# Kernel tuning notes

Measured on AMD Instinct MI355X. Metric: run time of the kernel, lower is better.

The kernel has to match this reference:

```python
import jax, jax.numpy as jnp
import numpy as np

EPS = 1e-6
H = 16  # num_heads

def _ln(x):
    mu = jnp.mean(x, axis=-1, keepdims=True)
    var = jnp.mean(jnp.square(x - mu), axis=-1, keepdims=True)
    return (x - mu) / jnp.sqrt(var + EPS)

def _mod(x, shift, scale):  # shift/scale: [B,D]
    return x * (1.0 + scale[:, None, :]) + shift[:, None, :]

def _heads(x, qkv_w, qkv_b):
    B, N, C = x.shape
    hd = C // H
    qkv = (x @ qkv_w + qkv_b).reshape(B, N, 3, H, hd).transpose(2, 0, 3, 1, 4)
    return qkv[0], qkv[1], qkv[2]  # each [B,H,N,hd]

def _attend(q, k, v):
    sc = (q.shape[-1]) ** -0.5
    a = jax.nn.softmax(jnp.einsum('bhnd,bhmd->bhnm', q, k) * sc, axis=-1)
    o = jnp.einsum('bhnm,bhmd->bhnd', a, v)
    B, h, N, hd = o.shape
    return o.transpose(0, 2, 1, 3).reshape(B, N, h * hd)

def _mha(x, qkv_w, qkv_b, proj_w, proj_b):
    q, k, v = _heads(x, qkv_w, qkv_b)
    return _attend(q, k, v) @ proj_w + proj_b

def setup_inputs() -> dict:
    key = jax.random.key(0)
    ks = jax.random.split(key, 16)
    B, T, D = 2, 2048, 1024
    Dh = 4 * D
    s = 0.02
    return {
        'x': jax.random.normal(ks[0], (B, T, D), jnp.float32),
        'c': jax.random.normal(ks[1], (B, 2, D), jnp.float32),
        'attn_qkv_w': jax.random.normal(ks[2], (D, 3 * D), jnp.float32) * s,
        'attn_qkv_b': jnp.zeros((3 * D,), jnp.float32),
        'attn_proj_w': jax.random.normal(ks[3], (D, D), jnp.float32) * s,
        'attn_proj_b': jnp.zeros((D,), jnp.float32),
        'crs_qkv_w': jax.random.normal(ks[4], (D, 3 * D), jnp.float32) * s,
        'crs_qkv_b': jnp.zeros((3 * D,), jnp.float32),
        'crs_proj_w': jax.random.normal(ks[5], (D, D), jnp.float32) * s,
        'crs_proj_b': jnp.zeros((D,), jnp.float32),
        'mlp_fc1_w': jax.random.normal(ks[6], (D, Dh), jnp.float32) * s,
        'mlp_fc1_b': jnp.zeros((Dh,), jnp.float32),
        'mlp_fc2_w': jax.random.normal(ks[7], (Dh, D), jnp.float32) * s,
        'mlp_fc2_b': jnp.zeros((D,), jnp.float32),
        'ada_w': jax.random.normal(ks[8], (D, 9 * D), jnp.float32) * s,
        'ada_b': jnp.zeros((9 * D,), jnp.float32),
    }

def reference(x, c, attn_qkv_w, attn_qkv_b, attn_proj_w, attn_proj_b,
              crs_qkv_w, crs_qkv_b, crs_proj_w, crs_proj_b,
              mlp_fc1_w, mlp_fc1_b, mlp_fc2_w, mlp_fc2_b, ada_w, ada_b):
    # adaLN-zero modulation: SiLU + Linear -> 9 chunks of [B,2,D]
    mod = jax.nn.silu(c) @ ada_w + ada_b
    (sh_msa, sc_msa, g_msa, sh_mca, sc_mca, g_mca,
     sh_mlp, sc_mlp, g_mlp) = jnp.split(mod, 9, axis=2)
    B, T, D = x.shape
    h = T // 2
    x0, x1 = x[:, :h], x[:, h:]
    # self-attention on each half with its own shift/scale/gate
    x0 = x0 + g_msa[:, 0][:, None, :] * _mha(_mod(_ln(x0), sh_msa[:, 0], sc_msa[:, 0]),
                                             attn_qkv_w, attn_qkv_b, attn_proj_w, attn_proj_b)
    x1 = x1 + g_msa[:, 1][:, None, :] * _mha(_mod(_ln(x1), sh_msa[:, 1], sc_msa[:, 1]),
                                             attn_qkv_w, attn_qkv_b, attn_proj_w, attn_proj_b)
    # two-way cross-attention
    xm = _mod(_ln(x0), sh_mca[:, 0], sc_mca[:, 0])
    ym = _mod(_ln(x1), sh_mca[:, 1], sc_mca[:, 1])
    qx, kx, vx = _heads(xm, crs_qkv_w, crs_qkv_b)
    qy, ky, vy = _heads(ym, crs_qkv_w, crs_qkv_b)
    ox = _attend(qx, ky, vy) @ crs_proj_w + crs_proj_b
    oy = _attend(qy, kx, vx) @ crs_proj_w + crs_proj_b
    x = x + jnp.concatenate((g_mca[:, 0][:, None, :] * ox,
                             g_mca[:, 1][:, None, :] * oy), axis=1)
    # gated MLP on each half
    def mlp(z):
        return jax.nn.gelu(z @ mlp_fc1_w + mlp_fc1_b, approximate=True) @ mlp_fc2_w + mlp_fc2_b
    m0 = mlp(_mod(_ln(x[:, :h]), sh_mlp[:, 0], sc_mlp[:, 0]))
    m1 = mlp(_mod(_ln(x[:, h:]), sh_mlp[:, 1], sc_mlp[:, 1]))
    x = x + jnp.concatenate((g_mlp[:, 0][:, None, :] * m0,
                             g_mlp[:, 1][:, None, :] * m1), axis=1)
    return x
```

## Files before the change

kernel.cpp:

```cpp
#include <hip/hip_runtime.h>
#include <hip/hip_bf16.h>

#define BB 2
#define TT 2048
#define DD 1024
#define NH 16
#define HALF 1024
#define DHID 4096
#define ND9 9216
#define ROWS (BB*TT)

using bf16 = __hip_bfloat16;
typedef short bf16x8 __attribute__((ext_vector_type(8)));
typedef float f32x4 __attribute__((ext_vector_type(4)));
typedef unsigned short u16;

__device__ __forceinline__ float bits2f(u16 b){ return __uint_as_float(((unsigned)b) << 16); }
__device__ __forceinline__ u16 fb(float v){
    unsigned u = __float_as_uint(v);
    u += 0x7fffu + ((u >> 16) & 1u);
    return (u16)(u >> 16);
}
__device__ __forceinline__ u16 fbh(float v){
    bf16 b = __float2bfloat16(v);
    return *(u16*)&b;
}
__device__ __forceinline__ float fexp2(float x){
#if __has_builtin(__builtin_amdgcn_exp2f)
    return __builtin_amdgcn_exp2f(x);
#else
    return exp2f(x);
#endif
}
__device__ __forceinline__ void gl_lds16(const u16* g, u16* l) {
    __builtin_amdgcn_global_load_lds(
        (const __attribute__((address_space(1))) unsigned int*)g,
        (__attribute__((address_space(3))) unsigned int*)l, 16, 0, 0);
}

__global__ void ada_part(const float* __restrict__ c, const float* __restrict__ ada_w,
                         float* __restrict__ part) {
    __shared__ float sc_[4][64];
    int s = blockIdx.y;
    int k0 = s * 64;
    int n0 = blockIdx.x * 1024 + threadIdx.x * 4;
    {
        int r = threadIdx.x >> 6, k = threadIdx.x & 63;
        float v = c[r*DD + k0 + k];
        sc_[r][k] = v / (1.f + __expf(-v));
    }
    __syncthreads();
    float4 a0 = {0,0,0,0}, a1 = {0,0,0,0}, a2 = {0,0,0,0}, a3 = {0,0,0,0};
    for (int k = 0; k < 64; ++k) {
        float4 wv = *(const float4*)&ada_w[(size_t)(k0 + k)*ND9 + n0];
        float s0 = sc_[0][k], s1 = sc_[1][k], s2 = sc_[2][k], s3 = sc_[3][k];
        a0.x += s0*wv.x; a0.y += s0*wv.y; a0.z += s0*wv.z; a0.w += s0*wv.w;
        a1.x += s1*wv.x; a1.y += s1*wv.y; a1.z += s1*wv.z; a1.w += s1*wv.w;
        a2.x += s2*wv.x; a2.y += s2*wv.y; a2.z += s2*wv.z; a2.w += s2*wv.w;
        a3.x += s3*wv.x; a3.y += s3*wv.y; a3.z += s3*wv.z; a3.w += s3*wv.w;
    }
    *(float4*)&part[((size_t)(s*4 + 0))*ND9 + n0] = a0;
    *(float4*)&part[((size_t)(s*4 + 1))*ND9 + n0] = a1;
    *(float4*)&part[((size_t)(s*4 + 2))*ND9 + n0] = a2;
    *(float4*)&part[((size_t)(s*4 + 3))*ND9 + n0] = a3;
}

__global__ void ada_reduce(const float* __restrict__ part, const float* __restrict__ ada_b,
                           float* __restrict__ mod) {
    int g = blockIdx.x * 1024 + threadIdx.x * 4;
    int r = g / ND9, n = g - r*ND9;
    float4 acc = *(const float4*)&ada_b[n];
    #pragma unroll
    for (int s = 0; s < 16; ++s) {
        float4 p = *(const float4*)&part[((size_t)(s*4 + r))*ND9 + n];
        acc.x += p.x; acc.y += p.y; acc.z += p.z; acc.w += p.w;
    }
    *(float4*)&mod[(size_t)r*ND9 + n] = acc;
}

__global__ void resid_ln(const float* __restrict__ src, const u16* __restrict__ gv,
                         const float* __restrict__ mod, int jshift, int jscale,
                         float* __restrict__ dstf, bf16* __restrict__ y) {
    int row = blockIdx.x;
    int b = row / TT, t = row % TT;
    int cz = (t >= HALF) ? 1 : 0;
    const float* mp = mod + (size_t)(b*2 + cz) * ND9;
    int tid = threadIdx.x;
    int w = tid >> 6, lane = tid & 63;
    int d0 = tid * 4;
    float4 s = *(const float4*)&src[(size_t)row*DD + d0];
    float v[4] = {s.x, s.y, s.z, s.w};
    if (gv) {
        ushort4 g = *(const ushort4*)&gv[(size_t)row*DD + d0];
        v[0] += bits2f(g.x); v[1] += bits2f(g.y); v[2] += bits2f(g.z); v[3] += bits2f(g.w);
    }
    if (dstf) *(float4*)&dstf[(size_t)row*DD + d0] = (float4){v[0], v[1], v[2], v[3]};
    float sum = v[0]+v[1]+v[2]+v[3];
    float ssq = v[0]*v[0]+v[1]*v[1]+v[2]*v[2]+v[3]*v[3];
    #pragma unroll
    for (int o = 32; o > 0; o >>= 1) {
        sum += __shfl_down(sum, o);
        ssq += __shfl_down(ssq, o);
    }
    __shared__ float wsum[4], wssq[4];
    if (lane == 0) { wsum[w] = sum; wssq[w] = ssq; }
    __syncthreads();
    float sall = (wsum[0]+wsum[1]) + (wsum[2]+wsum[3]);
    float qall = (wssq[0]+wssq[1]) + (wssq[2]+wssq[3]);
    float mean = sall * (1.f/DD);
    float var = qall * (1.f/DD) - mean*mean;
    float rstd = rsqrtf(var + 1e-6f);
    float4 sh = *(const float4*)&mp[jshift*DD + d0];
    float4 sc = *(const float4*)&mp[jscale*DD + d0];
    ushort4 o4;
    o4.x = fb((v[0]-mean)*rstd*(1.f+sc.x) + sh.x);
    o4.y = fb((v[1]-mean)*rstd*(1.f+sc.y) + sh.y);
    o4.z = fb((v[2]-mean)*rstd*(1.f+sc.z) + sh.z);
    o4.w = fb((v[3]-mean)*rstd*(1.f+sc.w) + sh.w);
    *(ushort4*)((u16*)y + (size_t)row*DD + d0) = o4;
}

__global__ void transpose_w(const float* __restrict__ W, u16* __restrict__ Wt, int K, int N) {
    __shared__ float T[32][33];
    int n0 = blockIdx.x * 32, k0 = blockIdx.y * 32;
    int lx = threadIdx.x & 31, ly = threadIdx.x >> 5;
    #pragma unroll
    for (int i = 0; i < 4; ++i)
        T[ly + i*8][lx] = W[(size_t)(k0 + ly + i*8)*N + n0 + lx];
    __syncthreads();
    #pragma unroll
    for (int i = 0; i < 4; ++i) {
        int n = ly + i*8;
        Wt[(size_t)(n0 + n)*K + k0 + lx] = fb(T[lx][n]);
    }
}

__global__ void vtrans(const u16* __restrict__ qkv, u16* __restrict__ vt) {
    __shared__ u16 T[64][72];
    int kt = blockIdx.y;
    int gh = blockIdx.x;
    int tid = threadIdx.x;
    int key = tid >> 2, c8 = (tid & 3) * 16;
    const u16* src = qkv + (size_t)((gh >> 4)*1024 + kt*64 + key)*3072 + 2048 + (gh & 15)*64 + c8;
    *(uint4*)&T[key][c8]     = *(const uint4*)src;
    *(uint4*)&T[key][c8 + 8] = *(const uint4*)(src + 8);
    __syncthreads();
    int d = tid >> 2, kc = (tid & 3) * 16;
    u16 tmp[16];
    #pragma unroll
    for (int i = 0; i < 16; ++i) tmp[i] = T[kc + i][d];
    u16* dst = vt + ((size_t)gh*64 + d)*1024 + kt*64 + kc;
    *(uint4*)&dst[0] = *(const uint4*)&tmp[0];
    *(uint4*)&dst[8] = *(const uint4*)&tmp[8];
}

__device__ __forceinline__ void epi_store(u16* out, int o_off, int N, int mm, int n, float v,
                                          const float* mod, int jg, int epi) {
    if (epi == 0) {
        out[(size_t)(mm - o_off)*N + n] = fb(v);
    } else if (epi == 1) {
        float z = 0.7978845608028654f*(v + 0.044715f*v*v*v);
        out[(size_t)(mm - o_off)*N + n] = fb(v / (1.f + __expf(-2.f*z)));
    } else {
        int brow = mm / TT, tt2 = mm % TT;
        int cz = (tt2 >= HALF) ? 1 : 0;
        const float* mp = mod + (size_t)(brow*2 + cz)*ND9 + (size_t)jg*DD;
        if (epi == 3) {
            out[(size_t)(mm - o_off)*N + n] = fb(mp[n]*v);
        } else {
            float* of = (float*)out;
            size_t idx = (size_t)(mm - o_off)*N + n;
            of[idx] += mp[n]*v;
        }
    }
}

__global__ __launch_bounds__(256, 2) void gemm_mfma(
    const u16* __restrict__ A, const u16* __restrict__ Wt, const float* __restrict__ bias,
    u16* __restrict__ out, const float* __restrict__ mod, int jg,
    int m_base, int a_off, int o_off, int K, int N, int epi)
{
    __shared__ u16 As[128*64];
    __shared__ u16 Bs[128*64];
    int tid = threadIdx.x;
    int w = tid >> 6, lane = tid & 63;
    int quad = lane >> 4, l16 = lane & 15;
    int m0 = m_base + blockIdx.y * 128;
    int n0 = blockIdx.x * 128;
    int wr = (w & 1) * 64, wc = (w >> 1) * 64;

    f32x4 acc[4][4];
    #pragma unroll
    for (int i = 0; i < 4; ++i)
        #pragma unroll
        for (int j = 0; j < 4; ++j) acc[i][j] = (f32x4){0.f,0.f,0.f,0.f};

    const u16* Ag = A + (size_t)(m0 - a_off) * K;
    const u16* Bg = Wt + (size_t)n0 * K;
    int srow = lane >> 3;
    int scol = (((lane & 7) ^ ((lane >> 3) & 7))) * 8;
    int xsw = (l16 & 7);

    for (int k0 = 0; k0 < K; k0 += 64) {
        #pragma unroll
        for (int c = 0; c < 4; ++c) {
            int ch = w*4 + c;
            gl_lds16(Ag + (size_t)(ch*8 + srow)*K + k0 + scol, As + ch*512);
            gl_lds16(Bg + (size_t)(ch*8 + srow)*K + k0 + scol, Bs + ch*512);
        }
        __syncthreads();
        #pragma unroll
        for (int kk = 0; kk < 2; ++kk) {
            int pc = ((kk*4 + quad) ^ xsw) * 8;
            bf16x8 af[4], bfr[4];
            #pragma unroll
            for (int i = 0; i < 4; ++i) af[i] = *(const bf16x8*)&As[(wr + i*16 + l16)*64 + pc];
            #pragma unroll
            for (int j = 0; j < 4; ++j) bfr[j] = *(const bf16x8*)&Bs[(wc + j*16 + l16)*64 + pc];
            #pragma unroll
            for (int i = 0; i < 4; ++i)
                #pragma unroll
                for (int j = 0; j < 4; ++j)
                    acc[i][j] = __builtin_amdgcn_mfma_f32_16x16x32_bf16(af[i], bfr[j], acc[i][j], 0, 0, 0);
        }
        __syncthreads();
    }

    #pragma unroll
    for (int i = 0; i < 4; ++i)
        #pragma unroll
        for (int r = 0; r < 4; ++r) {
            int mm = m0 + wr + i*16 + quad*4 + r;
            #pragma unroll
            for (int j = 0; j < 4; ++j) {
                int n = n0 + wc + j*16 + l16;
                epi_store(out, o_off, N, mm, n, acc[i][j][r] + bias[n], mod, jg, epi);
            }
        }
}

__global__ __launch_bounds__(256, 2) void gemm64(
    const u16* __restrict__ A, const u16* __restrict__ Wt, const float* __restrict__ bias,
    u16* __restrict__ out, const float* __restrict__ mod, int jg,
    int m_base, int a_off, int o_off, int K, int N, int epi)
{
    __shared__ u16 As[64*64];
    __shared__ u16 Bs[128*64];
    int tid = threadIdx.x;
    int w = tid >> 6, lane = tid & 63;
    int quad = lane >> 4, l16 = lane & 15;
    int m0 = m_base + blockIdx.y * 64;
    int n0 = blockIdx.x * 128;

    f32x4 acc[4][2];
    #pragma unroll
    for (int i = 0; i < 4; ++i)
        #pragma unroll
        for (int j = 0; j < 2; ++j) acc[i][j] = (f32x4){0.f,0.f,0.f,0.f};

    const u16* Ag = A + (size_t)(m0 - a_off) * K;
    const u16* Bg = Wt + (size_t)n0 * K;
    int srow = lane >> 3;
    int scol = (((lane & 7) ^ ((lane >> 3) & 7))) * 8;
    int xsw = (l16 & 7);

    for (int k0 = 0; k0 < K; k0 += 64) {
        #pragma unroll
        for (int c = 0; c < 2; ++c) {
            int ch = w*2 + c;
            gl_lds16(Ag + (size_t)(ch*8 + srow)*K + k0 + scol, As + ch*512);
        }
        #pragma unroll
        for (int c = 0; c < 4; ++c) {
            int ch = w*4 + c;
            gl_lds16(Bg + (size_t)(ch*8 + srow)*K + k0 + scol, Bs + ch*512);
        }
        __syncthreads();
        #pragma unroll
        for (int kk = 0; kk < 2; ++kk) {
            int pc = ((kk*4 + quad) ^ xsw) * 8;
            bf16x8 af[4], bfr[2];
            #pragma unroll
            for (int i = 0; i < 4; ++i) af[i] = *(const bf16x8*)&As[(i*16 + l16)*64 + pc];
            #pragma unroll
            for (int j = 0; j < 2; ++j) bfr[j] = *(const bf16x8*)&Bs[(w*32 + j*16 + l16)*64 + pc];
            #pragma unroll
            for (int i = 0; i < 4; ++i)
                #pragma unroll
                for (int j = 0; j < 2; ++j)
                    acc[i][j] = __builtin_amdgcn_mfma_f32_16x16x32_bf16(af[i], bfr[j], acc[i][j], 0, 0, 0);
        }
        __syncthreads();
    }

    #pragma unroll
    for (int i = 0; i < 4; ++i)
        #pragma unroll
        for (int r = 0; r < 4; ++r) {
            int mm = m0 + i*16 + quad*4 + r;
            #pragma unroll
            for (int j = 0; j < 2; ++j) {
                int n = n0 + w*32 + j*16 + l16;
                epi_store(out, o_off, N, mm, n, acc[i][j][r] + bias[n], mod, jg, epi);
            }
        }
}

__global__ __launch_bounds__(256) void attn_mfma(const u16* __restrict__ qkv,
                                                 const u16* __restrict__ vt,
                                                 u16* __restrict__ attn_out, int kv_swap) {
    __shared__ u16 Ks[2][64][72];
    __shared__ u16 Vs[2][64][72];
    __shared__ u16 Ps[4][16][72];
    int head = blockIdx.x, qt = blockIdx.y, bh = blockIdx.z;
    int kvbh = kv_swap ? (bh ^ 1) : bh;
    int tid = threadIdx.x;
    int w = tid >> 6, lane = tid & 63;
    int quad = lane >> 4, l16 = lane & 15;
    int qrow0 = bh*1024 + qt*64 + w*16;

    const u16* qp = qkv + (size_t)(qrow0 + l16)*3072 + head*64;
    bf16x8 qa0 = *(const bf16x8*)(qp + quad*8);
    bf16x8 qa1 = *(const bf16x8*)(qp + 32 + quad*8);

    f32x4 oacc[4];
    #pragma unroll
    for (int i = 0; i < 4; ++i) oacc[i] = (f32x4){0.f,0.f,0.f,0.f};
    float mst = -3e38f, lst = 0.f;

    int skey = tid >> 2, sc8 = (tid & 3) * 16;
    const u16* kbase = qkv + (size_t)(kvbh*1024 + skey)*3072 + 1024 + head*64 + sc8;
    const u16* vbase = vt + ((size_t)(kvbh*16 + head)*64 + skey)*1024 + sc8;

    uint4 kr0 = *(const uint4*)kbase;
    uint4 kr1 = *(const uint4*)(kbase + 8);
    uint4 vr0 = *(const uint4*)vbase;
    uint4 vr1 = *(const uint4*)(vbase + 8);
    *(uint4*)&Ks[0][skey][sc8]     = kr0;
    *(uint4*)&Ks[0][skey][sc8 + 8] = kr1;
    *(uint4*)&Vs[0][skey][sc8]     = vr0;
    *(uint4*)&Vs[0][skey][sc8 + 8] = vr1;
    __syncthreads();

    const float SSC = 0.125f * 1.4426950408889634f;
    int cur = 0;
    for (int kt = 0; kt < 16; ++kt) {
        if (kt < 15) {
            const u16* kp = kbase + (size_t)(kt + 1)*64*3072;
            kr0 = *(const uint4*)kp;
            kr1 = *(const uint4*)(kp + 8);
            const u16* vp = vbase + (kt + 1)*64;
            vr0 = *(const uint4*)vp;
            vr1 = *(const uint4*)(vp + 8);
        }

        f32x4 sacc[4];
        #pragma unroll
        for (int nt = 0; nt < 4; ++nt) sacc[nt] = (f32x4){0.f,0.f,0.f,0.f};
        __builtin_amdgcn_s_setprio(1);
        #pragma unroll
        for (int nt = 0; nt < 4; ++nt) {
            bf16x8 kb0 = *(const bf16x8*)&Ks[cur][nt*16 + l16][quad*8];
            bf16x8 kb1 = *(const bf16x8*)&Ks[cur][nt*16 + l16][32 + quad*8];
            sacc[nt] = __builtin_amdgcn_mfma_f32_16x16x32_bf16(kb0, qa0, sacc[nt], 0, 0, 0);
            sacc[nt] = __builtin_amdgcn_mfma_f32_16x16x32_bf16(kb1, qa1, sacc[nt], 0, 0, 0);
        }
        __builtin_amdgcn_s_setprio(0);

        float sv[4][4];
        float tm = -3e38f;
        #pragma unroll
        for (int nt = 0; nt < 4; ++nt)
            #pragma unroll
            for (int r = 0; r < 4; ++r) {
                sv[nt][r] = sacc[nt][r] * SSC;
                tm = fmaxf(tm, sv[nt][r]);
            }
        tm = fmaxf(tm, __shfl_xor(tm, 16));
        tm = fmaxf(tm, __shfl_xor(tm, 32));
        if (!__all(tm <= mst + 11.5f)) {
            float mnew = fmaxf(mst, tm);
            float alpha = fexp2(mst - mnew);
            lst *= alpha;
            #pragma unroll
            for (int dt = 0; dt < 4; ++dt)
                #pragma unroll
                for (int r = 0; r < 4; ++r) oacc[dt][r] *= alpha;
            mst = mnew;
        }
        float ls = 0.f;
        #pragma unroll
        for (int nt = 0; nt < 4; ++nt) {
            float p0 = fexp2(sv[nt][0] - mst), p1 = fexp2(sv[nt][1] - mst);
            float p2 = fexp2(sv[nt][2] - mst), p3 = fexp2(sv[nt][3] - mst);
            ls += (p0 + p1) + (p2 + p3);
            ushort4 pk = {fbh(p0), fbh(p1), fbh(p2), fbh(p3)};
            *(ushort4*)&Ps[w][l16][nt*16 + quad*4] = pk;
        }
        ls += __shfl_xor(ls, 16);
        ls += __shfl_xor(ls, 32);
        lst += ls;

        bf16x8 pa0 = *(const bf16x8*)&Ps[w][l16][quad*8];
        bf16x8 pa1 = *(const bf16x8*)&Ps[w][l16][32 + quad*8];
        __builtin_amdgcn_s_setprio(1);
        #pragma unroll
        for (int dt = 0; dt < 4; ++dt) {
            bf16x8 vb0 = *(const bf16x8*)&Vs[cur][dt*16 + l16][quad*8];
            bf16x8 vb1 = *(const bf16x8*)&Vs[cur][dt*16 + l16][32 + quad*8];
            oacc[dt] = __builtin_amdgcn_mfma_f32_16x16x32_bf16(vb0, pa0, oacc[dt], 0, 0, 0);
            oacc[dt] = __builtin_amdgcn_mfma_f32_16x16x32_bf16(vb1, pa1, oacc[dt], 0, 0, 0);
        }
        __builtin_amdgcn_s_setprio(0);

        if (kt < 15) {
            int nxt = cur ^ 1;
            *(uint4*)&Ks[nxt][skey][sc8]     = kr0;
            *(uint4*)&Ks[nxt][skey][sc8 + 8] = kr1;
            *(uint4*)&Vs[nxt][skey][sc8]     = vr0;
            *(uint4*)&Vs[nxt][skey][sc8 + 8] = vr1;
            __syncthreads();
            cur = nxt;
        }
    }
    float rl = 1.f / lst;
    #pragma unroll
    for (int dt = 0; dt < 4; ++dt) {
        ushort4 o4 = {fbh(oacc[dt][0]*rl), fbh(oacc[dt][1]*rl),
                      fbh(oacc[dt][2]*rl), fbh(oacc[dt][3]*rl)};
        *(ushort4*)&attn_out[(size_t)(qrow0 + l16)*DD + head*64 + dt*16 + quad*4] = o4;
    }
}

extern "C" void kernel_launch(void* const* d_in, const int* in_sizes, int n_in,
                              void* d_out, int out_size, void* d_ws, size_t ws_size,
                              hipStream_t stream) {
    const float* x          = (const float*)d_in[0];
    const float* c          = (const float*)d_in[1];
    const float* attn_qkv_w = (const float*)d_in[2];
    const float* attn_qkv_b = (const float*)d_in[3];
    const float* attn_proj_w= (const float*)d_in[4];
    const float* attn_proj_b= (const float*)d_in[5];
    const float* crs_qkv_w  = (const float*)d_in[6];
    const float* crs_qkv_b  = (const float*)d_in[7];
    const float* crs_proj_w = (const float*)d_in[8];
    const float* crs_proj_b = (const float*)d_in[9];
    const float* fc1_w      = (const float*)d_in[10];
    const float* fc1_b      = (const float*)d_in[11];
    const float* fc2_w      = (const float*)d_in[12];
    const float* fc2_b      = (const float*)d_in[13];
    const float* ada_w      = (const float*)d_in[14];
    const float* ada_b      = (const float*)d_in[15];
    float* out = (float*)d_out;

    char* ws = (char*)d_ws;
    float* mod = (float*)ws;
    char* R1   = ws + (256u<<10);
    char* Yr   = R1 + (16u<<20);
    char* AOr  = Yr + (8u<<20);
    char* BIGr = AOr + (8u<<20);

    u16*   wt_a  = (u16*)R1;
    u16*   vt    = (u16*)(R1 + (8u<<20));
    bf16*  y     = (bf16*)Yr;
    u16*   wt_p  = (u16*)Yr;
    u16*   attn_o= (u16*)AOr;
    u16*   big   = (u16*)BIGr;
    u16*   gvB   = (u16*)BIGr;
    u16*   hstage= (u16*)AOr;
    u16*   fc1_t = (u16*)R1;
    u16*   fc2_t = (u16*)(R1 + (8u<<20));
    float* apart = (float*)BIGr;

    ada_part<<<dim3(9, 16), 256, 0, stream>>>(c, ada_w, apart);
    ada_reduce<<<36, 256, 0, stream>>>(apart, ada_b, mod);

    transpose_w<<<dim3(3*DD/32, DD/32), 256, 0, stream>>>(attn_qkv_w, wt_a, DD, 3*DD);
    resid_ln<<<ROWS, 256, 0, stream>>>(x, nullptr, mod, 0, 1, out, y);
    gemm_mfma<<<dim3(3*DD/128, ROWS/128), 256, 0, stream>>>((const u16*)y, wt_a, attn_qkv_b,
                                                            big, nullptr, 0, 0, 0, 0, DD, 3*DD, 0);
    vtrans<<<dim3(64, 16), 256, 0, stream>>>(big, vt);
    attn_mfma<<<dim3(NH, 16, 4), 256, 0, stream>>>(big, vt, attn_o, 0);
    transpose_w<<<dim3(DD/32, DD/32), 256, 0, stream>>>(attn_proj_w, wt_p, DD, DD);
    gemm64<<<dim3(DD/128, ROWS/64), 256, 0, stream>>>(attn_o, wt_p, attn_proj_b,
                                                      gvB, mod, 2, 0, 0, 0, DD, DD, 3);
    resid_ln<<<ROWS, 256, 0, stream>>>(out, gvB, mod, 3, 4, nullptr, y);

    transpose_w<<<dim3(3*DD/32, DD/32), 256, 0, stream>>>(crs_qkv_w, wt_a, DD, 3*DD);
    gemm_mfma<<<dim3(3*DD/128, ROWS/128), 256, 0, stream>>>((const u16*)y, wt_a, crs_qkv_b,
                                                            big, nullptr, 0, 0, 0, 0, DD, 3*DD, 0);
    vtrans<<<dim3(64, 16), 256, 0, stream>>>(big, vt);
    attn_mfma<<<dim3(NH, 16, 4), 256, 0, stream>>>(big, vt, attn_o, 1);
    transpose_w<<<dim3(DD/32, DD/32), 256, 0, stream>>>(crs_proj_w, wt_p, DD, DD);
    gemm64<<<dim3(DD/128, ROWS/64), 256, 0, stream>>>(attn_o, wt_p, crs_proj_b,
                                                      gvB, mod, 5, 0, 0, 0, DD, DD, 3);
    resid_ln<<<ROWS, 256, 0, stream>>>(out, gvB, mod, 6, 7, out, y);

    transpose_w<<<dim3(DHID/32, DD/32), 256, 0, stream>>>(fc1_w, fc1_t, DD, DHID);
    transpose_w<<<dim3(DD/32, DHID/32), 256, 0, stream>>>(fc2_w, fc2_t, DHID, DD);
    gemm_mfma<<<dim3(DHID/128, ROWS/128), 256, 0, stream>>>((const u16*)y, fc1_t, fc1_b,
                                                            hstage, nullptr, 0, 0, 0, 0, DD, DHID, 1);
    gemm64<<<dim3(DD/128, ROWS/64), 256, 0, stream>>>(hstage, fc2_t, fc2_b,
                                                      (u16*)out, mod, 8, 0, 0, 0, DHID, DD, 4);
}
```

Baseline: 549.1 us.

## Read attention K/V straight from global, deepen gemm64 K-step, drop unused offsets

The attention kernel no longer double-buffers K and V tiles through shared memory with a barrier per tile. Each wave now loads its MFMA operands directly from global memory (relying on cache), which removes LDS traffic and syncs but drops both the software prefetch and the sharing of tiles across the four waves. The 64-row projection GEMM now stages a 128-wide K slab per iteration, halving the number of barriers. The unused m_base/a_off/o_off parameters are removed from both GEMMs.

```diff
diff --git a/kernel.cpp b/kernel.cpp
--- a/kernel.cpp
+++ b/kernel.cpp
@@ -154,22 +154,22 @@
     *(uint4*)&dst[8] = *(const uint4*)&tmp[8];
 }
 
-__device__ __forceinline__ void epi_store(u16* out, int o_off, int N, int mm, int n, float v,
+__device__ __forceinline__ void epi_store(u16* out, int N, int mm, int n, float v,
                                           const float* mod, int jg, int epi) {
     if (epi == 0) {
-        out[(size_t)(mm - o_off)*N + n] = fb(v);
+        out[(size_t)mm*N + n] = fb(v);
     } else if (epi == 1) {
         float z = 0.7978845608028654f*(v + 0.044715f*v*v*v);
-        out[(size_t)(mm - o_off)*N + n] = fb(v / (1.f + __expf(-2.f*z)));
+        out[(size_t)mm*N + n] = fb(v / (1.f + __expf(-2.f*z)));
     } else {
         int brow = mm / TT, tt2 = mm % TT;
         int cz = (tt2 >= HALF) ? 1 : 0;
         const float* mp = mod + (size_t)(brow*2 + cz)*ND9 + (size_t)jg*DD;
         if (epi == 3) {
-            out[(size_t)(mm - o_off)*N + n] = fb(mp[n]*v);
+            out[(size_t)mm*N + n] = fb(mp[n]*v);
         } else {
             float* of = (float*)out;
-            size_t idx = (size_t)(mm - o_off)*N + n;
+            size_t idx = (size_t)mm*N + n;
             of[idx] += mp[n]*v;
         }
     }
@@ -178,14 +178,14 @@
 __global__ __launch_bounds__(256, 2) void gemm_mfma(
     const u16* __restrict__ A, const u16* __restrict__ Wt, const float* __restrict__ bias,
     u16* __restrict__ out, const float* __restrict__ mod, int jg,
-    int m_base, int a_off, int o_off, int K, int N, int epi)
+    int K, int N, int epi)
 {
     __shared__ u16 As[128*64];
     __shared__ u16 Bs[128*64];
     int tid = threadIdx.x;
     int w = tid >> 6, lane = tid & 63;
     int quad = lane >> 4, l16 = lane & 15;
-    int m0 = m_base + blockIdx.y * 128;
+    int m0 = blockIdx.y * 128;
     int n0 = blockIdx.x * 128;
     int wr = (w & 1) * 64, wc = (w >> 1) * 64;
 
@@ -195,7 +195,7 @@
         #pragma unroll
         for (int j = 0; j < 4; ++j) acc[i][j] = (f32x4){0.f,0.f,0.f,0.f};
 
-    const u16* Ag = A + (size_t)(m0 - a_off) * K;
+    const u16* Ag = A + (size_t)m0 * K;
     const u16* Bg = Wt + (size_t)n0 * K;
     int srow = lane >> 3;
     int scol = (((lane & 7) ^ ((lane >> 3) & 7))) * 8;
@@ -234,22 +234,22 @@
             #pragma unroll
             for (int j = 0; j < 4; ++j) {
                 int n = n0 + wc + j*16 + l16;
-                epi_store(out, o_off, N, mm, n, acc[i][j][r] + bias[n], mod, jg, epi);
+                epi_store(out, N, mm, n, acc[i][j][r] + bias[n], mod, jg, epi);
             }
         }
 }
 
-__global__ __launch_bounds__(256, 2) void gemm64(
+__global__ __launch_bounds__(256, 2) void gemm64_k128(
     const u16* __restrict__ A, const u16* __restrict__ Wt, const float* __restrict__ bias,
     u16* __restrict__ out, const float* __restrict__ mod, int jg,
-    int m_base, int a_off, int o_off, int K, int N, int epi)
+    int K, int N, int epi)
 {
-    __shared__ u16 As[64*64];
-    __shared__ u16 Bs[128*64];
+    __shared__ u16 As[2*64*64];
+    __shared__ u16 Bs[2*128*64];
     int tid = threadIdx.x;
     int w = tid >> 6, lane = tid & 63;
     int quad = lane >> 4, l16 = lane & 15;
-    int m0 = m_base + blockIdx.y * 64;
+    int m0 = blockIdx.y * 64;
     int n0 = blockIdx.x * 128;
 
     f32x4 acc[4][2];
@@ -258,32 +258,36 @@
         #pragma unroll
         for (int j = 0; j < 2; ++j) acc[i][j] = (f32x4){0.f,0.f,0.f,0.f};
 
-    const u16* Ag = A + (size_t)(m0 - a_off) * K;
+    const u16* Ag = A + (size_t)m0 * K;
     const u16* Bg = Wt + (size_t)n0 * K;
     int srow = lane >> 3;
     int scol = (((lane & 7) ^ ((lane >> 3) & 7))) * 8;
     int xsw = (l16 & 7);
 
-    for (int k0 = 0; k0 < K; k0 += 64) {
-        #pragma unroll
-        for (int c = 0; c < 2; ++c) {
-            int ch = w*2 + c;
-            gl_lds16(Ag + (size_t)(ch*8 + srow)*K + k0 + scol, As + ch*512);
-        }
-        #pragma unroll
-        for (int c = 0; c < 4; ++c) {
-            int ch = w*4 + c;
-            gl_lds16(Bg + (size_t)(ch*8 + srow)*K + k0 + scol, Bs + ch*512);
+    for (int k0 = 0; k0 < K; k0 += 128) {
+        #pragma unroll
+        for (int h = 0; h < 2; ++h) {
+            #pragma unroll
+            for (int c = 0; c < 2; ++c) {
+                int ch = w*2 + c;
+                gl_lds16(Ag + (size_t)(ch*8 + srow)*K + k0 + h*64 + scol, As + h*4096 + ch*512);
+            }
+            #pragma unroll
+            for (int c = 0; c < 4; ++c) {
+                int ch = w*4 + c;
+                gl_lds16(Bg + (size_t)(ch*8 + srow)*K + k0 + h*64 + scol, Bs + h*8192 + ch*512);
+            }
         }
         __syncthreads();
         #pragma unroll
-        for (int kk = 0; kk < 2; ++kk) {
-            int pc = ((kk*4 + quad) ^ xsw) * 8;
+        for (int kk = 0; kk < 4; ++kk) {
+            int hh = kk >> 1;
+            int pc = (((kk & 1)*4 + quad) ^ xsw) * 8;
             bf16x8 af[4], bfr[2];
             #pragma unroll
-            for (int i = 0; i < 4; ++i) af[i] = *(const bf16x8*)&As[(i*16 + l16)*64 + pc];
-            #pragma unroll
-            for (int j = 0; j < 2; ++j) bfr[j] = *(const bf16x8*)&Bs[(w*32 + j*16 + l16)*64 + pc];
+            for (int i = 0; i < 4; ++i) af[i] = *(const bf16x8*)&As[hh*4096 + (i*16 + l16)*64 + pc];
+            #pragma unroll
+            for (int j = 0; j < 2; ++j) bfr[j] = *(const bf16x8*)&Bs[hh*8192 + (w*32 + j*16 + l16)*64 + pc];
             #pragma unroll
             for (int i = 0; i < 4; ++i)
                 #pragma unroll
@@ -301,7 +305,7 @@
             #pragma unroll
             for (int j = 0; j < 2; ++j) {
                 int n = n0 + w*32 + j*16 + l16;
-                epi_store(out, o_off, N, mm, n, acc[i][j][r] + bias[n], mod, jg, epi);
+                epi_store(out, N, mm, n, acc[i][j][r] + bias[n], mod, jg, epi);
             }
         }
 }
@@ -309,8 +313,6 @@
 __global__ __launch_bounds__(256) void attn_mfma(const u16* __restrict__ qkv,
                                                  const u16* __restrict__ vt,
                                                  u16* __restrict__ attn_out, int kv_swap) {
-    __shared__ u16 Ks[2][64][72];
-    __shared__ u16 Vs[2][64][72];
     __shared__ u16 Ps[4][16][72];
     int head = blockIdx.x, qt = blockIdx.y, bh = blockIdx.z;
     int kvbh = kv_swap ? (bh ^ 1) : bh;
@@ -328,40 +330,20 @@
     for (int i = 0; i < 4; ++i) oacc[i] = (f32x4){0.f,0.f,0.f,0.f};
     float mst = -3e38f, lst = 0.f;
 
-    int skey = tid >> 2, sc8 = (tid & 3) * 16;
-    const u16* kbase = qkv + (size_t)(kvbh*1024 + skey)*3072 + 1024 + head*64 + sc8;
-    const u16* vbase = vt + ((size_t)(kvbh*16 + head)*64 + skey)*1024 + sc8;
-
-    uint4 kr0 = *(const uint4*)kbase;
-    uint4 kr1 = *(const uint4*)(kbase + 8);
-    uint4 vr0 = *(const uint4*)vbase;
-    uint4 vr1 = *(const uint4*)(vbase + 8);
-    *(uint4*)&Ks[0][skey][sc8]     = kr0;
-    *(uint4*)&Ks[0][skey][sc8 + 8] = kr1;
-    *(uint4*)&Vs[0][skey][sc8]     = vr0;
-    *(uint4*)&Vs[0][skey][sc8 + 8] = vr1;
-    __syncthreads();
+    const u16* kptr = qkv + (size_t)(kvbh*1024 + l16)*3072 + 1024 + head*64 + quad*8;
+    const u16* vptr = vt + ((size_t)(kvbh*16 + head)*64 + l16)*1024 + quad*8;
 
     const float SSC = 0.125f * 1.4426950408889634f;
-    int cur = 0;
     for (int kt = 0; kt < 16; ++kt) {
-        if (kt < 15) {
-            const u16* kp = kbase + (size_t)(kt + 1)*64*3072;
-            kr0 = *(const uint4*)kp;
-            kr1 = *(const uint4*)(kp + 8);
-            const u16* vp = vbase + (kt + 1)*64;
-            vr0 = *(const uint4*)vp;
-            vr1 = *(const uint4*)(vp + 8);
-        }
-
+        const u16* kp = kptr + (size_t)kt*64*3072;
         f32x4 sacc[4];
         #pragma unroll
         for (int nt = 0; nt < 4; ++nt) sacc[nt] = (f32x4){0.f,0.f,0.f,0.f};
         __builtin_amdgcn_s_setprio(1);
         #pragma unroll
         for (int nt = 0; nt < 4; ++nt) {
-            bf16x8 kb0 = *(const bf16x8*)&Ks[cur][nt*16 + l16][quad*8];
-            bf16x8 kb1 = *(const bf16x8*)&Ks[cur][nt*16 + l16][32 + quad*8];
+            bf16x8 kb0 = *(const bf16x8*)(kp + (size_t)nt*16*3072);
+            bf16x8 kb1 = *(const bf16x8*)(kp + (size_t)nt*16*3072 + 32);
             sacc[nt] = __builtin_amdgcn_mfma_f32_16x16x32_bf16(kb0, qa0, sacc[nt], 0, 0, 0);
             sacc[nt] = __builtin_amdgcn_mfma_f32_16x16x32_bf16(kb1, qa1, sacc[nt], 0, 0, 0);
         }
@@ -403,25 +385,16 @@
 
         bf16x8 pa0 = *(const bf16x8*)&Ps[w][l16][quad*8];
         bf16x8 pa1 = *(const bf16x8*)&Ps[w][l16][32 + quad*8];
+        const u16* vp = vptr + kt*64;
         __builtin_amdgcn_s_setprio(1);
         #pragma unroll
         for (int dt = 0; dt < 4; ++dt) {
-            bf16x8 vb0 = *(const bf16x8*)&Vs[cur][dt*16 + l16][quad*8];
-            bf16x8 vb1 = *(const bf16x8*)&Vs[cur][dt*16 + l16][32 + quad*8];
+            bf16x8 vb0 = *(const bf16x8*)(vp + (size_t)dt*16*1024);
+            bf16x8 vb1 = *(const bf16x8*)(vp + (size_t)dt*16*1024 + 32);
             oacc[dt] = __builtin_amdgcn_mfma_f32_16x16x32_bf16(vb0, pa0, oacc[dt], 0, 0, 0);
             oacc[dt] = __builtin_amdgcn_mfma_f32_16x16x32_bf16(vb1, pa1, oacc[dt], 0, 0, 0);
         }
         __builtin_amdgcn_s_setprio(0);
-
-        if (kt < 15) {
-            int nxt = cur ^ 1;
-            *(uint4*)&Ks[nxt][skey][sc8]     = kr0;
-            *(uint4*)&Ks[nxt][skey][sc8 + 8] = kr1;
-            *(uint4*)&Vs[nxt][skey][sc8]     = vr0;
-            *(uint4*)&Vs[nxt][skey][sc8 + 8] = vr1;
-            __syncthreads();
-            cur = nxt;
-        }
     }
     float rl = 1.f / lst;
     #pragma unroll
@@ -478,28 +451,28 @@
     transpose_w<<<dim3(3*DD/32, DD/32), 256, 0, stream>>>(attn_qkv_w, wt_a, DD, 3*DD);
     resid_ln<<<ROWS, 256, 0, stream>>>(x, nullptr, mod, 0, 1, out, y);
     gemm_mfma<<<dim3(3*DD/128, ROWS/128), 256, 0, stream>>>((const u16*)y, wt_a, attn_qkv_b,
-                                                            big, nullptr, 0, 0, 0, 0, DD, 3*DD, 0);
+                                                            big, nullptr, 0, DD, 3*DD, 0);
     vtrans<<<dim3(64, 16), 256, 0, stream>>>(big, vt);
     attn_mfma<<<dim3(NH, 16, 4), 256, 0, stream>>>(big, vt, attn_o, 0);
     transpose_w<<<dim3(DD/32, DD/32), 256, 0, stream>>>(attn_proj_w, wt_p, DD, DD);
-    gemm64<<<dim3(DD/128, ROWS/64), 256, 0, stream>>>(attn_o, wt_p, attn_proj_b,
-                                                      gvB, mod, 2, 0, 0, 0, DD, DD, 3);
+    gemm64_k128<<<dim3(DD/128, ROWS/64), 256, 0, stream>>>(attn_o, wt_p, attn_proj_b,
+                                                           gvB, mod, 2, DD, DD, 3);
     resid_ln<<<ROWS, 256, 0, stream>>>(out, gvB, mod, 3, 4, nullptr, y);
 
     transpose_w<<<dim3(3*DD/32, DD/32), 256, 0, stream>>>(crs_qkv_w, wt_a, DD, 3*DD);
     gemm_mfma<<<dim3(3*DD/128, ROWS/128), 256, 0, stream>>>((const u16*)y, wt_a, crs_qkv_b,
-                                                            big, nullptr, 0, 0, 0, 0, DD, 3*DD, 0);
+                                                            big, nullptr, 0, DD, 3*DD, 0);
     vtrans<<<dim3(64, 16), 256, 0, stream>>>(big, vt);
     attn_mfma<<<dim3(NH, 16, 4), 256, 0, stream>>>(big, vt, attn_o, 1);
     transpose_w<<<dim3(DD/32, DD/32), 256, 0, stream>>>(crs_proj_w, wt_p, DD, DD);
-    gemm64<<<dim3(DD/128, ROWS/64), 256, 0, stream>>>(attn_o, wt_p, crs_proj_b,
-                                                      gvB, mod, 5, 0, 0, 0, DD, DD, 3);
+    gemm64_k128<<<dim3(DD/128, ROWS/64), 256, 0, stream>>>(attn_o, wt_p, crs_proj_b,
+                                                           gvB, mod, 5, DD, DD, 3);
     resid_ln<<<ROWS, 256, 0, stream>>>(out, gvB, mod, 6, 7, out, y);
 
     transpose_w<<<dim3(DHID/32, DD/32), 256, 0, stream>>>(fc1_w, fc1_t, DD, DHID);
     transpose_w<<<dim3(DD/32, DHID/32), 256, 0, stream>>>(fc2_w, fc2_t, DHID, DD);
     gemm_mfma<<<dim3(DHID/128, ROWS/128), 256, 0, stream>>>((const u16*)y, fc1_t, fc1_b,
-                                                            hstage, nullptr, 0, 0, 0, 0, DD, DHID, 1);
-    gemm64<<<dim3(DD/128, ROWS/64), 256, 0, stream>>>(hstage, fc2_t, fc2_b,
-                                                      (u16*)out, mod, 8, 0, 0, 0, DHID, DD, 4);
-}
+                                                            hstage, nullptr, 0, DD, DHID, 1);
+    gemm64_k128<<<dim3(DD/128, ROWS/64), 256, 0, stream>>>(hstage, fc2_t, fc2_b,
+                                                           (u16*)out, mod, 8, DHID, DD, 4);
+}
```

After: 687.6 us. 25.2% more time.
